# Performance work log

Measured on AMD Instinct MI355X. Metric: run time of the kernel, lower is better.

## Reference

```python
import jax, jax.numpy as jnp
import numpy as np

F = 32          # conf['num_features']
G = 96          # voxel grid extent
N_VOX = 80000   # occupied input voxels
BN_EPS = 1e-5


def _encode(c):
    c = c.astype(np.int64) + 8
    return (c[:, 0] * 512 + c[:, 1]) * 512 + c[:, 2]


def _offsets(ks, dil):
    r = np.arange(-(ks // 2), ks // 2 + 1) * dil
    return np.stack(np.meshgrid(r, r, r, indexing='ij'), -1).reshape(-1, 3)


def _build_map(in_coords, out_coords, offsets):
    # For each kernel offset k and output voxel j, find input voxel index at
    # out_coords[j] + offsets[k]; sentinel = n_in / n_out when absent.
    n_in, n_out = len(in_coords), len(out_coords)
    keys = _encode(in_coords)
    order = np.argsort(keys).astype(np.int32)
    skeys = keys[order]
    K = len(offsets)
    in_map = np.full((K, n_out), n_in, np.int32)
    out_map = np.full((K, n_out), n_out, np.int32)
    base = np.arange(n_out, dtype=np.int32)
    for k, off in enumerate(offsets):
        q = _encode(out_coords + off)
        pos = np.clip(np.searchsorted(skeys, q), 0, n_in - 1)
        valid = skeys[pos] == q
        in_map[k] = np.where(valid, order[pos], n_in)
        out_map[k] = np.where(valid, base, n_out)
    return jnp.asarray(in_map), jnp.asarray(out_map)


def setup_inputs() -> dict:
    rng = np.random.default_rng(0)
    idx = rng.choice(G ** 3, size=N_VOX, replace=False)
    coords = np.stack(np.unravel_index(idx, (G, G, G)), 1).astype(np.int64)
    c2 = np.unique(coords // 2 * 2, axis=0)   # stride-2 coords (enc1 output)
    c4 = np.unique(coords // 4 * 4, axis=0)   # stride-4 coords (c_out.C)

    m1_in, m1_out = _build_map(coords, c2, _offsets(5, 1))  # k5 s2 conv
    m2_in, m2_out = _build_map(c2, c2, _offsets(3, 2))      # enc1 blocks
    m3_in, m3_out = _build_map(c2, c4, _offsets(3, 2))      # conv2 -> c_out.C
    m4_in, m4_out = _build_map(c4, c4, _offsets(3, 4))      # enc2 blocks

    key = jax.random.key(0)
    ks = jax.random.split(key, 8)
    s = 0.05
    return {
        'x_geo': jax.random.normal(ks[0], (N_VOX, 1), jnp.float32),
        'x_col': jax.random.uniform(ks[1], (N_VOX, 3), jnp.float32),
        'w0': jax.random.normal(ks[2], (125, 4, F), jnp.float32) * s,
        'w_e1': jax.random.normal(ks[3], (2, 2, 27, F, F), jnp.float32) * s,
        'g_e1': jnp.ones((2, 2, F), jnp.float32),
        'b_e1': jnp.zeros((2, 2, F), jnp.float32),
        'w2': jax.random.normal(ks[4], (27, F, 2 * F), jnp.float32) * s,
        'w_e2': jax.random.normal(ks[5], (2, 2, 27, 2 * F, 2 * F), jnp.float32) * s,
        'g_e2': jnp.ones((2, 2, 2 * F), jnp.float32),
        'b_e2': jnp.zeros((2, 2, 2 * F), jnp.float32),
        'm1_in': m1_in, 'm1_out': m1_out,
        'm2_in': m2_in, 'm2_out': m2_out,
        'm3_in': m3_in, 'm3_out': m3_out,
        'm4_in': m4_in, 'm4_out': m4_out,
    }


def sparse_conv(feats, W, in_map, out_map):
    # gather -> GEMM -> scatter per kernel offset (lax.scan over K offsets)
    n_out = out_map.shape[1]
    fpad = jnp.concatenate([feats, jnp.zeros((1, feats.shape[1]), feats.dtype)], 0)
    out0 = jnp.zeros((n_out + 1, W.shape[2]), feats.dtype)
    def step(acc, kmw):
        im, om, w = kmw
        return acc.at[om].add(fpad[im] @ w), None
    out, _ = jax.lax.scan(step, out0, (in_map, out_map, W))
    return out[:n_out]


def batch_norm(x, g, b):
    mu = x.mean(0)
    var = ((x - mu) ** 2).mean(0)
    return (x - mu) * jax.lax.rsqrt(var + BN_EPS) * g + b


def basic_block(x, w, g, b, in_map, out_map):
    # ME BasicBlock: conv-BN-ReLU-conv-BN + residual, ReLU
    y = jax.nn.relu(batch_norm(sparse_conv(x, w[0], in_map, out_map), g[0], b[0]))
    y = batch_norm(sparse_conv(y, w[1], in_map, out_map), g[1], b[1])
    return jax.nn.relu(y + x)


def reference(x_geo, x_col, w0, w_e1, g_e1, b_e1, w2, w_e2, g_e2, b_e2,
              m1_in, m1_out, m2_in, m2_out, m3_in, m3_out, m4_in, m4_out):
    x = jnp.concatenate([x_geo, x_col], axis=1)          # ME.cat -> 4 channels
    x = jax.nn.relu(sparse_conv(x, w0, m1_in, m1_out))   # k5 s2 conv + ReLU
    for i in range(2):                                   # enc1 residual blocks
        x = basic_block(x, w_e1[i], g_e1[i], b_e1[i], m2_in, m2_out)
    x = sparse_conv(x, w2, m3_in, m3_out)                # conv2 onto c_out.C
    for i in range(2):                                   # enc2 residual blocks
        x = basic_block(x, w_e2[i], g_e2[i], b_e2[i], m4_in, m4_out)
    return x
```

## Files before the change

kernel.cpp:

```cpp
#include <hip/hip_runtime.h>
#include <hip/hip_bf16.h>


typedef float f4 __attribute__((ext_vector_type(4)));
typedef short short8 __attribute__((ext_vector_type(8)));
typedef short short4v __attribute__((ext_vector_type(4)));

#define BN_EPS 1e-5f

static inline int ceil_div(int a, int b) { return (a + b - 1) / b; }

static __device__ inline float btof(short s) {
    unsigned u = ((unsigned)(unsigned short)s) << 16;
    float f;
    __builtin_memcpy(&f, &u, 4);
    return f;
}
static __device__ inline short ftob(float f) {
    __hip_bfloat16 h = __float2bfloat16(f);
    short s;
    __builtin_memcpy(&s, &h, 2);
    return s;
}

static __device__ inline int xcd_swz(int b, int nwg) {
    int q = nwg >> 3, rr = nwg & 7;
    int xcd = b & 7, pos = b >> 3;
    return (xcd < rr) ? (xcd * (q + 1) + pos)
                      : (rr * (q + 1) + (xcd - rr) * q + pos);
}

static __device__ inline void gl_lds16(const void* g, void* l) {
    __builtin_amdgcn_global_load_lds(
        (const __attribute__((address_space(1))) void*)g,
        (__attribute__((address_space(3))) void*)l, 16, 0, 0);
}

template <int N>
static __device__ inline void s_wait_vmcnt() {
    static_assert(N >= 0 && N <= 20, "vmcnt range");
    if constexpr (N == 0) asm volatile("s_waitcnt vmcnt(0)" ::: "memory");
    else if constexpr (N == 8) asm volatile("s_waitcnt vmcnt(8)" ::: "memory");
    else if constexpr (N == 9) asm volatile("s_waitcnt vmcnt(9)" ::: "memory");
    else if constexpr (N == 18) asm volatile("s_waitcnt vmcnt(18)" ::: "memory");
    else if constexpr (N == 6) asm volatile("s_waitcnt vmcnt(6)" ::: "memory");
    else asm volatile("s_waitcnt vmcnt(4)" ::: "memory");
}

struct Seg {
    const float* W;
    long long begin, end;
    int K, CIN, COUT;
};

struct ProArgs {
    Seg s[10];
    const float* geo;
    const float* col;
    __hip_bfloat16* x0;
    int n_vox;
    float* stats;
    __hip_bfloat16* pads[5];
    int padn[5];
    long long wf_total;
    long long pro_total;
    __hip_bfloat16* Wf;
    const int* m1;
    __hip_bfloat16* A;
    int nc2;
};

template <int C>
__device__ inline void bn_coef(const float* st, const float* g, const float* b,
                               int c, int n, float& sc, float& sh) {
    constexpr int NS = (C == 32) ? 8 : 4;
    float rn = 1.f / (float)n;
    float sum = 0.f, sq = 0.f;
#pragma unroll
    for (int s = 0; s < NS; ++s) {
        sum += st[(s * 2 + 0) * C + c];
        sq  += st[(s * 2 + 1) * C + c];
    }
    float mu = sum * rn;
    float inv = rsqrtf(sq * rn - mu * mu + BN_EPS);
    sc = inv * g[c];
    sh = b[c] - mu * sc;
}

__global__ __launch_bounds__(256) void k_prologue(ProArgs pa) {
    for (long long e = (long long)blockIdx.x * 256 + threadIdx.x; e < pa.pro_total;
         e += (long long)gridDim.x * 256) {
        if (e < pa.wf_total) {
            int si = 0;
#pragma unroll
            for (int i = 0; i < 10; ++i)
                if (e >= pa.s[i].end) si = i + 1;
            const Seg sg = pa.s[si];
            long long r = e - sg.begin;
            int j = (int)(r & 7);
            int lane = (int)((r >> 3) & 63);
            long long rest = r >> 9;
            int NT = sg.COUT >> 4;
            int ntile = (int)(rest % NT);
            int chunk = (int)(rest / NT);
            int kd = chunk * 32 + ((lane >> 4) << 3) + j;
            int koff = kd / sg.CIN;
            int ci = kd % sg.CIN;
            int n = ntile * 16 + (lane & 15);
            float v = (koff < sg.K) ? sg.W[((size_t)koff * sg.CIN + ci) * sg.COUT + n] : 0.f;
            pa.Wf[e] = __float2bfloat16(v);
            continue;
        }
        long long r = e - pa.wf_total;
        if (r < pa.n_vox) {
            int row = (int)r;
            pa.x0[row * 4 + 0] = __float2bfloat16(pa.geo[row]);
            pa.x0[row * 4 + 1] = __float2bfloat16(pa.col[row * 3 + 0]);
            pa.x0[row * 4 + 2] = __float2bfloat16(pa.col[row * 3 + 1]);
            pa.x0[row * 4 + 3] = __float2bfloat16(pa.col[row * 3 + 2]);
            continue;
        }
        r -= pa.n_vox;
        if (r < 4096) {
            pa.stats[r] = 0.f;
            continue;
        }
        r -= 4096;
#pragma unroll
        for (int i = 0; i < 5; ++i) {
            if (r < pa.padn[i]) {
                pa.pads[i][r] = __float2bfloat16(0.f);
                r = -1;
                break;
            }
            r -= pa.padn[i];
        }
    }
}

__global__ __launch_bounds__(256) void k_stem(ProArgs a) {
    const int t = threadIdx.x, w = t >> 6, lane = t & 63;
    const int quad = lane >> 4, ml = lane & 15;
    const int ntile = w & 1, mgroup = w >> 1;
    const int n_out = a.nc2, n_in = a.n_vox;
    const __hip_bfloat16* feat = a.x0;
    const __hip_bfloat16* Wf = a.Wf;
    const int* in_map = a.m1;
    __hip_bfloat16* out = a.A;
    const int mb = blockIdx.x * 64 + mgroup * 32;
    const int m0 = mb + ml, m1 = mb + 16 + ml;
    const bool v0 = m0 < n_out, v1 = m1 < n_out;
    f4 acc0 = {0.f, 0.f, 0.f, 0.f};
    f4 acc1 = {0.f, 0.f, 0.f, 0.f};
#pragma unroll 2
    for (int chunk = 0; chunk < 16; ++chunk) {
        int k0 = chunk * 8 + quad * 2;
        int k1 = k0 + 1;
        int k0c = (k0 < 125) ? k0 : 0;
        int k1c = (k1 < 125) ? k1 : 0;
        short8 b = *(const short8*)(Wf + ((size_t)(chunk * 2 + ntile) * 64 + lane) * 8);
        int ia = v0 ? in_map[(size_t)k0c * n_out + m0] : n_in;
        int ib = v0 ? in_map[(size_t)k1c * n_out + m0] : n_in;
        int ic = v1 ? in_map[(size_t)k0c * n_out + m1] : n_in;
        int id = v1 ? in_map[(size_t)k1c * n_out + m1] : n_in;
        short4v p0 = *(const short4v*)(feat + (size_t)ia * 4);
        short4v p1 = *(const short4v*)(feat + (size_t)ib * 4);
        short4v p2 = *(const short4v*)(feat + (size_t)ic * 4);
        short4v p3 = *(const short4v*)(feat + (size_t)id * 4);
        short8 a0, a1;
        a0[0] = p0[0]; a0[1] = p0[1]; a0[2] = p0[2]; a0[3] = p0[3];
        a0[4] = p1[0]; a0[5] = p1[1]; a0[6] = p1[2]; a0[7] = p1[3];
        a1[0] = p2[0]; a1[1] = p2[1]; a1[2] = p2[2]; a1[3] = p2[3];
        a1[4] = p3[0]; a1[5] = p3[1]; a1[6] = p3[2]; a1[7] = p3[3];
        acc0 = __builtin_amdgcn_mfma_f32_16x16x32_bf16(a0, b, acc0, 0, 0, 0);
        acc1 = __builtin_amdgcn_mfma_f32_16x16x32_bf16(a1, b, acc1, 0, 0, 0);
    }
    const int col = ntile * 16 + ml;
#pragma unroll
    for (int i = 0; i < 4; ++i) {
        int r0 = mb + quad * 4 + i;
        if (r0 < n_out)
            out[(size_t)r0 * 32 + col] = __float2bfloat16(fmaxf(acc0[i], 0.f));
        int r1 = mb + 16 + quad * 4 + i;
        if (r1 < n_out)
            out[(size_t)r1 * 32 + col] = __float2bfloat16(fmaxf(acc1[i], 0.f));
    }
}

template <int CIN, int COUT, int MT, int K, bool BNF>
__global__ __launch_bounds__(256, (CIN == 64) ? 3 : 4)
void k_conv(
    const __hip_bfloat16* __restrict__ feat,
    const __hip_bfloat16* __restrict__ Wf,
    const int* __restrict__ in_map,
    __hip_bfloat16* __restrict__ out,
    float* __restrict__ stats,
    const float* __restrict__ in_stats,
    const float* __restrict__ in_g,
    const float* __restrict__ in_b,
    int n_out, int n_in) {
    constexpr int NT = COUT / 16;
    constexpr int H = CIN / 32;
    constexpr int R = MT * 16;
    constexpr int KPW = (K + 3) / 4;
    constexpr int SP = COUT + 1;
    constexpr int S = CIN / 8;
    constexpr int SW = (S == 4) ? 1 : 0;
    constexpr int RPI = 64 / S;
    constexpr int NI = R / RPI;
    constexpr int NB = H * NT;
    constexpr int D = 2;
    constexpr int WAIT_N = NI + 2 * NB;
    constexpr int NSLOT = (COUT == 32) ? 8 : 4;
    constexpr int STAGE_B = R * CIN * 2;
    constexpr int STAGE_TOT = 4 * D * STAGE_B;
    constexpr int RED_B = 4 * R * SP * 4;
    constexpr int UNION_B = (STAGE_TOT > RED_B) ? STAGE_TOT : RED_B;

    __shared__ char smem[UNION_B + 2048 + 512];
    float* red  = (float*)smem;
    float* sred = (float*)(smem + UNION_B);
    float* ibn  = (float*)(smem + UNION_B + 2048);

    const int t = threadIdx.x, w = t >> 6, lane = t & 63;
    const int quad = lane >> 4, ml = lane & 15;
    const int wb = xcd_swz((int)blockIdx.x, (int)gridDim.x);
    const int mb = wb * R;
    char* stw = smem + w * (D * STAGE_B);
    const int srow = lane / S;
    const int ssl = lane & (S - 1);

    if constexpr (BNF) {
        if (t < CIN) {
            float sc, sh;
            bn_coef<CIN>(in_stats, in_g, in_b, t, n_in, sc, sh);
            ibn[t] = sc;
            ibn[CIN + t] = sh;
        }
        __syncthreads();
    }
    float scr[H][8], shr[H][8];
    if constexpr (BNF) {
#pragma unroll
        for (int h = 0; h < H; ++h)
#pragma unroll
            for (int j = 0; j < 8; ++j) {
                int ch = h * 32 + quad * 8 + j;
                scr[h][j] = ibn[ch];
                shr[h][j] = ibn[CIN + ch];
            }
    }

    int idxs[KPW][NI];
#pragma unroll
    for (int kk = 0; kk < KPW; ++kk) {
        const int k = kk * 4 + w;
        const int krow = (k < K) ? k : 0;
        const int* mk = in_map + (size_t)krow * n_out;
#pragma unroll
        for (int inst = 0; inst < NI; ++inst) {
            int m = mb + inst * RPI + srow;
            idxs[kk][inst] = (m < n_out) ? mk[m] : n_in;
        }
    }

    f4 acc[MT * NT];
#pragma unroll
    for (int i = 0; i < MT * NT; ++i) acc[i] = (f4){0.f, 0.f, 0.f, 0.f};

    short8 bf0[NB], bf1[NB];

    auto issue_stage = [&](int stg, int slot) {
#pragma unroll
        for (int inst = 0; inst < NI; ++inst) {
            int rg = inst * RPI + srow;
            int gsl = ssl ^ ((rg >> SW) & (S - 1));
            const __hip_bfloat16* src =
                feat + (size_t)idxs[stg][inst] * CIN + gsl * 8;
            gl_lds16(src, stw + slot * STAGE_B + inst * 1024);
        }
    };
    auto issue_bf = [&](int stg, short8 (&bfc)[NB]) {
        const int k = stg * 4 + w;
#pragma unroll
        for (int h = 0; h < H; ++h)
#pragma unroll
            for (int nt = 0; nt < NT; ++nt)
                bfc[h * NT + nt] = *(const short8*)(
                    Wf + (((size_t)(k * H + h) * NT + nt) * 64 + lane) * 8);
    };

    issue_stage(0, 0);
    issue_bf(0, bf0);
    issue_stage(1, 1);
    issue_bf(1, bf1);
    __builtin_amdgcn_sched_barrier(0);

#pragma unroll
    for (int kk = 0; kk < KPW; ++kk) {
        s_wait_vmcnt<WAIT_N>();
        __builtin_amdgcn_sched_barrier(0);

        const int slot = kk & 1;
        short8 (&bfc)[NB] = (kk & 1) ? bf1 : bf0;

        int cidx[MT];
        if constexpr (BNF) {
#pragma unroll
            for (int mi = 0; mi < MT; ++mi) {
                if constexpr (RPI >= 16) {
                    cidx[mi] = __shfl(idxs[kk][(mi * 16) / RPI], ml * S);
                } else {
                    int a0 = __shfl(idxs[kk][0], (ml & 7) * S);
                    int a1 = __shfl(idxs[kk][NI - 1], (ml & 7) * S);
                    cidx[mi] = (ml < 8) ? a0 : a1;
                }
            }
        }

#pragma unroll
        for (int mi = 0; mi < MT; ++mi) {
#pragma unroll
            for (int h = 0; h < H; ++h) {
                const int p = (h * 4 + quad) ^ ((ml >> SW) & (S - 1));
                short8 a = *(const short8*)(
                    stw + slot * STAGE_B + ((mi * 16 + ml) * CIN + p * 8) * 2);
                if constexpr (BNF) {
                    const bool sent = (cidx[mi] == n_in);
#pragma unroll
                    for (int j = 0; j < 8; ++j) {
                        float f = btof(a[j]) * scr[h][j] + shr[h][j];
                        f = fmaxf(f, 0.f);
                        a[j] = sent ? (short)0 : ftob(f);
                    }
                }
#pragma unroll
                for (int nt = 0; nt < NT; ++nt)
                    acc[mi * NT + nt] = __builtin_amdgcn_mfma_f32_16x16x32_bf16(
                        a, bfc[h * NT + nt], acc[mi * NT + nt], 0, 0, 0);
            }
        }

        __builtin_amdgcn_sched_barrier(0);
        const int ns = (kk + 2 < KPW) ? (kk + 2) : 0;
        issue_stage(ns, slot);
        if (kk & 1) issue_bf(ns, bf1); else issue_bf(ns, bf0);
        __builtin_amdgcn_sched_barrier(0);
    }

#pragma unroll
    for (int i = 0; i < NB; ++i) {
        asm volatile("" ::"v"(bf0[i]));
        asm volatile("" ::"v"(bf1[i]));
    }

    s_wait_vmcnt<0>();
    __syncthreads();

#pragma unroll
    for (int mi = 0; mi < MT; ++mi)
#pragma unroll
        for (int nt = 0; nt < NT; ++nt)
#pragma unroll
            for (int i = 0; i < 4; ++i)
                red[((size_t)w * R + mi * 16 + quad * 4 + i) * SP + nt * 16 + ml] =
                    acc[mi * NT + nt][i];
    __syncthreads();

    constexpr int E = (R * COUT) / 256;
    constexpr int RSTEP = 256 / COUT;
    const int col = t % COUT;
    const int rg = t / COUT;
    float s = 0.f, s2 = 0.f;
#pragma unroll
    for (int i = 0; i < E; ++i) {
        int r = rg + i * RSTEP;
        float v = red[(0 * R + r) * SP + col] + red[(1 * R + r) * SP + col] +
                  red[(2 * R + r) * SP + col] + red[(3 * R + r) * SP + col];
        s += v;
        s2 += v * v;
        int grow = mb + r;
        if (grow < n_out) out[(size_t)grow * COUT + col] = __float2bfloat16(v);
    }

    if (stats) {
        sred[t] = s;
        sred[256 + t] = s2;
        __syncthreads();
        if (t < 2 * COUT) {
            int c = t % COUT;
            int which = t / COUT;
            float v = 0.f;
#pragma unroll
            for (int j = 0; j < RSTEP; ++j) v += sred[which * 256 + j * COUT + c];
            atomicAdd(&stats[((wb & (NSLOT - 1)) * 2 + which) * COUT + c], v);
        }
    }
}

template <int C, bool F32OUT>
__global__ __launch_bounds__(256) void k_bnres(
    const __hip_bfloat16* __restrict__ y, const __hip_bfloat16* __restrict__ res,
    const float* __restrict__ st, const float* __restrict__ g,
    const float* __restrict__ b, void* outp, int n) {
    __shared__ float ibn[2 * C];
    const int t = threadIdx.x;
    if (t < C) {
        float sc, sh;
        bn_coef<C>(st, g, b, t, n, sc, sh);
        ibn[t] = sc;
        ibn[C + t] = sh;
    }
    __syncthreads();
    long long tot = (long long)n * (C / 8);
    long long i = (long long)blockIdx.x * 256 + t;
    if (i >= tot) return;
    int c0 = (int)(i % (C / 8)) * 8;
    short8 v = *(const short8*)(y + i * 8);
    short8 r = *(const short8*)(res + i * 8);
    if constexpr (F32OUT) {
        float* out = (float*)outp;
        f4 o0, o1;
#pragma unroll
        for (int j = 0; j < 8; ++j) {
            float f = btof(v[j]) * ibn[c0 + j] + ibn[C + c0 + j] + btof(r[j]);
            f = fmaxf(f, 0.f);
            if (j < 4) o0[j] = f; else o1[j - 4] = f;
        }
        *(f4*)(out + i * 8) = o0;
        *(f4*)(out + i * 8 + 4) = o1;
    } else {
        __hip_bfloat16* out = (__hip_bfloat16*)outp;
        short8 o;
#pragma unroll
        for (int j = 0; j < 8; ++j) {
            float f = btof(v[j]) * ibn[c0 + j] + ibn[C + c0 + j] + btof(r[j]);
            o[j] = ftob(fmaxf(f, 0.f));
        }
        *(short8*)(out + i * 8) = o;
    }
}

extern "C" void kernel_launch(void* const* d_in, const int* in_sizes, int n_in_cnt,
                              void* d_out, int out_size, void* d_ws, size_t ws_size,
                              hipStream_t stream) {
    const float* x_geo = (const float*)d_in[0];
    const float* x_col = (const float*)d_in[1];
    const float* w0    = (const float*)d_in[2];
    const float* w_e1  = (const float*)d_in[3];
    const float* g_e1  = (const float*)d_in[4];
    const float* b_e1  = (const float*)d_in[5];
    const float* w2    = (const float*)d_in[6];
    const float* w_e2  = (const float*)d_in[7];
    const float* g_e2  = (const float*)d_in[8];
    const float* b_e2  = (const float*)d_in[9];
    const int* m1 = (const int*)d_in[10];
    const int* m2 = (const int*)d_in[12];
    const int* m3 = (const int*)d_in[14];
    const int* m4 = (const int*)d_in[16];

    const int n_vox = in_sizes[0];
    const int nc2 = in_sizes[10] / 125;
    const int nc4 = in_sizes[14] / 27;
    (void)out_size; (void)ws_size; (void)n_in_cnt;

    char* p = (char*)d_ws;
    auto alloc = [&](size_t bytes) -> char* {
        char* r = p;
        p += (bytes + 255) & ~(size_t)255;
        return r;
    };
    float* stats = (float*)alloc(8 * 512 * sizeof(float));
    __hip_bfloat16* x0 = (__hip_bfloat16*)alloc((size_t)(n_vox + 1) * 4 * 2);
    __hip_bfloat16* A  = (__hip_bfloat16*)alloc((size_t)(nc2 + 1) * 32 * 2);
    __hip_bfloat16* B  = (__hip_bfloat16*)alloc((size_t)(nc2 + 1) * 32 * 2);
    __hip_bfloat16* Cb = (__hip_bfloat16*)alloc((size_t)(nc2 + 1) * 32 * 2);
    __hip_bfloat16* D  = (__hip_bfloat16*)alloc((size_t)(nc4 + 1) * 64 * 2);
    __hip_bfloat16* E  = (__hip_bfloat16*)alloc((size_t)(nc4 + 1) * 64 * 2);
    __hip_bfloat16* Fb = (__hip_bfloat16*)alloc((size_t)(nc4 + 1) * 64 * 2);

    const long long sz_stem = 16LL * 2 * 512;
    const long long sz_e1   = 28LL * 2 * 512;
    const long long sz_c2   = 28LL * 4 * 512;
    const long long sz_e2   = 56LL * 4 * 512;
    const long long wf_total = sz_stem + 4 * sz_e1 + sz_c2 + 4 * sz_e2;
    __hip_bfloat16* Wf = (__hip_bfloat16*)alloc((size_t)wf_total * 2);

    ProArgs pa;
    long long cur = 0;
    auto seg = [&](int i, const float* W, int K, int CIN, int COUT, long long n) {
        pa.s[i].W = W; pa.s[i].K = K; pa.s[i].CIN = CIN; pa.s[i].COUT = COUT;
        pa.s[i].begin = cur; pa.s[i].end = cur + n; cur += n;
    };
    seg(0, w0, 125, 4, 32, sz_stem);
    for (int i = 0; i < 4; ++i)
        seg(1 + i, w_e1 + (size_t)i * 27 * 32 * 32, 27, 32, 32, sz_e1);
    seg(5, w2, 27, 32, 64, sz_c2);
    for (int i = 0; i < 4; ++i)
        seg(6 + i, w_e2 + (size_t)i * 27 * 64 * 64, 27, 64, 64, sz_e2);

    long long off_e1[4], off_e2[4];
    cur = sz_stem;
    for (int i = 0; i < 4; ++i) { off_e1[i] = cur; cur += sz_e1; }
    long long off_c2 = cur; cur += sz_c2;
    for (int i = 0; i < 4; ++i) { off_e2[i] = cur; cur += sz_e2; }

    pa.geo = x_geo; pa.col = x_col; pa.x0 = x0; pa.n_vox = n_vox;
    pa.stats = stats;
    pa.pads[0] = x0 + (size_t)n_vox * 4; pa.padn[0] = 4;
    pa.pads[1] = A + (size_t)nc2 * 32;   pa.padn[1] = 32;
    pa.pads[2] = B + (size_t)nc2 * 32;   pa.padn[2] = 32;
    pa.pads[3] = D + (size_t)nc4 * 64;   pa.padn[3] = 64;
    pa.pads[4] = E + (size_t)nc4 * 64;   pa.padn[4] = 64;
    pa.wf_total = wf_total;
    pa.pro_total = wf_total + n_vox + 4096 + (4 + 32 + 32 + 64 + 64);
    pa.Wf = Wf;
    pa.m1 = m1;
    pa.A = A;
    pa.nc2 = nc2;

    k_prologue<<<ceil_div((int)pa.pro_total, 256), 256, 0, stream>>>(pa);
    k_stem<<<ceil_div(nc2, 64), 256, 0, stream>>>(pa);

    k_conv<32, 32, 4, 27, false><<<ceil_div(nc2, 64), 256, 0, stream>>>(
        A, Wf + off_e1[0], m2, B, stats + 0 * 512,
        nullptr, nullptr, nullptr, nc2, nc2);
    k_conv<32, 32, 4, 27, true><<<ceil_div(nc2, 64), 256, 0, stream>>>(
        B, Wf + off_e1[1], m2, Cb, stats + 1 * 512,
        stats + 0 * 512, g_e1 + 0, b_e1 + 0, nc2, nc2);
    k_bnres<32, false><<<ceil_div(nc2 * 4, 256), 256, 0, stream>>>(
        Cb, A, stats + 1 * 512, g_e1 + 32, b_e1 + 32, A, nc2);

    k_conv<32, 32, 4, 27, false><<<ceil_div(nc2, 64), 256, 0, stream>>>(
        A, Wf + off_e1[2], m2, B, stats + 2 * 512,
        nullptr, nullptr, nullptr, nc2, nc2);
    k_conv<32, 32, 4, 27, true><<<ceil_div(nc2, 64), 256, 0, stream>>>(
        B, Wf + off_e1[3], m2, Cb, stats + 3 * 512,
        stats + 2 * 512, g_e1 + 64, b_e1 + 64, nc2, nc2);
    k_bnres<32, false><<<ceil_div(nc2 * 4, 256), 256, 0, stream>>>(
        Cb, A, stats + 3 * 512, g_e1 + 96, b_e1 + 96, A, nc2);

    k_conv<32, 64, 1, 27, false><<<ceil_div(nc4, 16), 256, 0, stream>>>(
        A, Wf + off_c2, m3, D, nullptr,
        nullptr, nullptr, nullptr, nc4, nc2);

    k_conv<64, 64, 1, 27, false><<<ceil_div(nc4, 16), 256, 0, stream>>>(
        D, Wf + off_e2[0], m4, E, stats + 4 * 512,
        nullptr, nullptr, nullptr, nc4, nc4);
    k_conv<64, 64, 1, 27, true><<<ceil_div(nc4, 16), 256, 0, stream>>>(
        E, Wf + off_e2[1], m4, Fb, stats + 5 * 512,
        stats + 4 * 512, g_e2 + 0, b_e2 + 0, nc4, nc4);
    k_bnres<64, false><<<ceil_div(nc4 * 8, 256), 256, 0, stream>>>(
        Fb, D, stats + 5 * 512, g_e2 + 64, b_e2 + 64, D, nc4);

    k_conv<64, 64, 1, 27, false><<<ceil_div(nc4, 16), 256, 0, stream>>>(
        D, Wf + off_e2[2], m4, E, stats + 6 * 512,
        nullptr, nullptr, nullptr, nc4, nc4);
    k_conv<64, 64, 1, 27, true><<<ceil_div(nc4, 16), 256, 0, stream>>>(
        E, Wf + off_e2[3], m4, Fb, stats + 7 * 512,
        stats + 6 * 512, g_e2 + 128, b_e2 + 128, nc4, nc4);
    k_bnres<64, true><<<ceil_div(nc4 * 8, 256), 256, 0, stream>>>(
        Fb, D, stats + 7 * 512, g_e2 + 192, b_e2 + 192, (float*)d_out, nc4);
}
```

Before: 306.9 us.

## Add hybrid LDS/register gather schedule for MT=4 enc1 conv; shift-based prologue indexing

For the enc1 conv shape (MT==4), kernel offsets now alternate between two paths. Even stages gather rows into LDS with global_load_lds, and odd stages load rows straight into registers in MFMA layout, with a deeper prefetch of four steps ahead. The aim is to cut LDS staging traffic and hide gather latency better, at the cost of more VGPRs; occupancy is lowered to 3 waves for this shape. The prologue weight reformat also replaces integer div/mod with shifts and masks, using log2 fields added per segment.

New measurement: 320.3 us. 4.4% more time.

```diff
diff --git a/kernel.cpp b/kernel.cpp
--- a/kernel.cpp
+++ b/kernel.cpp
@@ -38,19 +38,19 @@
 
 template <int N>
 static __device__ inline void s_wait_vmcnt() {
-    static_assert(N >= 0 && N <= 20, "vmcnt range");
     if constexpr (N == 0) asm volatile("s_waitcnt vmcnt(0)" ::: "memory");
+    else if constexpr (N == 6) asm volatile("s_waitcnt vmcnt(6)" ::: "memory");
+    else if constexpr (N == 9) asm volatile("s_waitcnt vmcnt(9)" ::: "memory");
+    else if constexpr (N == 14) asm volatile("s_waitcnt vmcnt(14)" ::: "memory");
+    else if constexpr (N == 18) asm volatile("s_waitcnt vmcnt(18)" ::: "memory");
     else if constexpr (N == 8) asm volatile("s_waitcnt vmcnt(8)" ::: "memory");
-    else if constexpr (N == 9) asm volatile("s_waitcnt vmcnt(9)" ::: "memory");
-    else if constexpr (N == 18) asm volatile("s_waitcnt vmcnt(18)" ::: "memory");
-    else if constexpr (N == 6) asm volatile("s_waitcnt vmcnt(6)" ::: "memory");
     else asm volatile("s_waitcnt vmcnt(4)" ::: "memory");
 }
 
 struct Seg {
     const float* W;
     long long begin, end;
-    int K, CIN, COUT;
+    int K, CIN, COUT, lgc, lgnt;
 };
 
 struct ProArgs {
@@ -100,12 +100,11 @@
             int j = (int)(r & 7);
             int lane = (int)((r >> 3) & 63);
             long long rest = r >> 9;
-            int NT = sg.COUT >> 4;
-            int ntile = (int)(rest % NT);
-            int chunk = (int)(rest / NT);
+            int ntile = (int)(rest & ((1 << sg.lgnt) - 1));
+            int chunk = (int)(rest >> sg.lgnt);
             int kd = chunk * 32 + ((lane >> 4) << 3) + j;
-            int koff = kd / sg.CIN;
-            int ci = kd % sg.CIN;
+            int koff = kd >> sg.lgc;
+            int ci = kd & (sg.CIN - 1);
             int n = ntile * 16 + (lane & 15);
             float v = (koff < sg.K) ? sg.W[((size_t)koff * sg.CIN + ci) * sg.COUT + n] : 0.f;
             pa.Wf[e] = __float2bfloat16(v);
@@ -188,7 +187,7 @@
 }
 
 template <int CIN, int COUT, int MT, int K, bool BNF>
-__global__ __launch_bounds__(256, (CIN == 64) ? 3 : 4)
+__global__ __launch_bounds__(256, (CIN == 64 || MT == 4) ? 3 : 4)
 void k_conv(
     const __hip_bfloat16* __restrict__ feat,
     const __hip_bfloat16* __restrict__ Wf,
@@ -216,6 +215,9 @@
     constexpr int STAGE_TOT = 4 * D * STAGE_B;
     constexpr int RED_B = 4 * R * SP * 4;
     constexpr int UNION_B = (STAGE_TOT > RED_B) ? STAGE_TOT : RED_B;
+    constexpr bool HYB = (MT == 4);
+    static_assert(!HYB || (NI == 4 && NB == 2 && H == 1 && KPW == 7),
+                  "hybrid schedule assumes enc1 shape");
 
     __shared__ char smem[UNION_B + 2048 + 512];
     float* red  = (float*)smem;
@@ -251,111 +253,250 @@
             }
     }
 
-    int idxs[KPW][NI];
-#pragma unroll
-    for (int kk = 0; kk < KPW; ++kk) {
-        const int k = kk * 4 + w;
-        const int krow = (k < K) ? k : 0;
-        const int* mk = in_map + (size_t)krow * n_out;
-#pragma unroll
-        for (int inst = 0; inst < NI; ++inst) {
-            int m = mb + inst * RPI + srow;
-            idxs[kk][inst] = (m < n_out) ? mk[m] : n_in;
-        }
-    }
-
     f4 acc[MT * NT];
 #pragma unroll
     for (int i = 0; i < MT * NT; ++i) acc[i] = (f4){0.f, 0.f, 0.f, 0.f};
 
-    short8 bf0[NB], bf1[NB];
-
-    auto issue_stage = [&](int stg, int slot) {
-#pragma unroll
-        for (int inst = 0; inst < NI; ++inst) {
-            int rg = inst * RPI + srow;
-            int gsl = ssl ^ ((rg >> SW) & (S - 1));
-            const __hip_bfloat16* src =
-                feat + (size_t)idxs[stg][inst] * CIN + gsl * 8;
-            gl_lds16(src, stw + slot * STAGE_B + inst * 1024);
-        }
-    };
-    auto issue_bf = [&](int stg, short8 (&bfc)[NB]) {
-        const int k = stg * 4 + w;
-#pragma unroll
-        for (int h = 0; h < H; ++h)
+    if constexpr (HYB) {
+        int sidx[4][NI];
+        int vidx[3][MT];
+#pragma unroll
+        for (int e = 0; e < 4; ++e) {
+            const int k = (2 * e) * 4 + w;
+            const int krow = (k < K) ? k : 0;
+            const int* mk = in_map + (size_t)krow * n_out;
+#pragma unroll
+            for (int inst = 0; inst < NI; ++inst) {
+                int m = mb + inst * RPI + srow;
+                sidx[e][inst] = (m < n_out) ? mk[m] : n_in;
+            }
+        }
+#pragma unroll
+        for (int o = 0; o < 3; ++o) {
+            const int k = (2 * o + 1) * 4 + w;
+            const int krow = (k < K) ? k : 0;
+            const int* mk = in_map + (size_t)krow * n_out;
+#pragma unroll
+            for (int mi = 0; mi < MT; ++mi) {
+                int m = mb + mi * 16 + ml;
+                vidx[o][mi] = (m < n_out) ? mk[m] : n_in;
+            }
+        }
+
+        short8 vs0[MT], vs1[MT];
+        short8 bf0[NB], bf1[NB];
+
+        auto issue_S = [&](int e, int slot) {
+#pragma unroll
+            for (int inst = 0; inst < NI; ++inst) {
+                int rg = inst * RPI + srow;
+                int gsl = ssl ^ ((rg >> SW) & (S - 1));
+                const __hip_bfloat16* src =
+                    feat + (size_t)sidx[e][inst] * CIN + gsl * 8;
+                gl_lds16(src, stw + slot * STAGE_B + inst * 1024);
+            }
+        };
+        auto issue_V = [&](int o, short8 (&vs)[MT]) {
+#pragma unroll
+            for (int mi = 0; mi < MT; ++mi)
+                vs[mi] = *(const short8*)(
+                    feat + (size_t)vidx[o][mi] * CIN + quad * 8);
+        };
+        auto issue_B = [&](int kk, short8 (&bfc)[NB]) {
+            const int k = kk * 4 + w;
+#pragma unroll
+            for (int h = 0; h < H; ++h)
+#pragma unroll
+                for (int nt = 0; nt < NT; ++nt)
+                    bfc[h * NT + nt] = *(const short8*)(
+                        Wf + (((size_t)(k * H + h) * NT + nt) * 64 + lane) * 8);
+        };
+        auto mfma_row = [&](int mi, short8 a, short8 (&bfc)[NB], bool sent) {
+            if constexpr (BNF) {
+#pragma unroll
+                for (int j = 0; j < 8; ++j) {
+                    float f = btof(a[j]) * scr[0][j] + shr[0][j];
+                    f = fmaxf(f, 0.f);
+                    a[j] = sent ? (short)0 : ftob(f);
+                }
+            }
+            (void)sent;
 #pragma unroll
             for (int nt = 0; nt < NT; ++nt)
-                bfc[h * NT + nt] = *(const short8*)(
-                    Wf + (((size_t)(k * H + h) * NT + nt) * 64 + lane) * 8);
-    };
-
-    issue_stage(0, 0);
-    issue_bf(0, bf0);
-    issue_stage(1, 1);
-    issue_bf(1, bf1);
-    __builtin_amdgcn_sched_barrier(0);
-
-#pragma unroll
-    for (int kk = 0; kk < KPW; ++kk) {
-        s_wait_vmcnt<WAIT_N>();
+                acc[mi * NT + nt] = __builtin_amdgcn_mfma_f32_16x16x32_bf16(
+                    a, bfc[nt], acc[mi * NT + nt], 0, 0, 0);
+        };
+
+        issue_S(0, 0);
+        issue_B(0, bf0);
+        issue_V(0, vs0);
+        issue_B(1, bf1);
+        issue_S(1, 1);
+        issue_V(1, vs1);
         __builtin_amdgcn_sched_barrier(0);
 
-        const int slot = kk & 1;
-        short8 (&bfc)[NB] = (kk & 1) ? bf1 : bf0;
-
-        int cidx[MT];
-        if constexpr (BNF) {
-#pragma unroll
-            for (int mi = 0; mi < MT; ++mi) {
-                if constexpr (RPI >= 16) {
-                    cidx[mi] = __shfl(idxs[kk][(mi * 16) / RPI], ml * S);
-                } else {
-                    int a0 = __shfl(idxs[kk][0], (ml & 7) * S);
-                    int a1 = __shfl(idxs[kk][NI - 1], (ml & 7) * S);
-                    cidx[mi] = (ml < 8) ? a0 : a1;
+#pragma unroll
+        for (int kk = 0; kk < 7; ++kk) {
+            if (kk < 2) s_wait_vmcnt<14>(); else s_wait_vmcnt<6>();
+            __builtin_amdgcn_sched_barrier(0);
+
+            if ((kk & 1) == 0) {
+                const int e = kk >> 1;
+                const int slot = e & 1;
+                int cidx[MT];
+                if constexpr (BNF) {
+#pragma unroll
+                    for (int mi = 0; mi < MT; ++mi)
+                        cidx[mi] = __shfl(sidx[e][mi], ml * S);
                 }
-            }
-        }
-
-#pragma unroll
-        for (int mi = 0; mi < MT; ++mi) {
-#pragma unroll
-            for (int h = 0; h < H; ++h) {
-                const int p = (h * 4 + quad) ^ ((ml >> SW) & (S - 1));
-                short8 a = *(const short8*)(
-                    stw + slot * STAGE_B + ((mi * 16 + ml) * CIN + p * 8) * 2);
-                if constexpr (BNF) {
-                    const bool sent = (cidx[mi] == n_in);
-#pragma unroll
-                    for (int j = 0; j < 8; ++j) {
-                        float f = btof(a[j]) * scr[h][j] + shr[h][j];
-                        f = fmaxf(f, 0.f);
-                        a[j] = sent ? (short)0 : ftob(f);
+#pragma unroll
+                for (int mi = 0; mi < MT; ++mi) {
+                    const int p = quad ^ ((ml >> SW) & (S - 1));
+                    short8 a = *(const short8*)(
+                        stw + slot * STAGE_B + ((mi * 16 + ml) * CIN + p * 8) * 2);
+                    bool sent = false;
+                    if constexpr (BNF) sent = (cidx[mi] == n_in);
+                    if (kk & 1) mfma_row(mi, a, bf1, sent);
+                    else        mfma_row(mi, a, bf0, sent);
+                }
+            } else {
+                const int o = kk >> 1;
+#pragma unroll
+                for (int mi = 0; mi < MT; ++mi) {
+                    short8 a = (o & 1) ? vs1[mi] : vs0[mi];
+                    bool sent = false;
+                    if constexpr (BNF) sent = (vidx[o][mi] == n_in);
+                    mfma_row(mi, a, bf1, sent);
+                }
+            }
+
+            __builtin_amdgcn_sched_barrier(0);
+            const int nk = kk + 4;
+            if ((nk & 1) == 0) {
+                issue_S((nk <= 6) ? (nk >> 1) : 0, (nk >> 1) & 1);
+            } else {
+                const int no = (nk <= 5) ? (nk >> 1) : 0;
+                if ((nk >> 1) & 1) issue_V(no, vs1); else issue_V(no, vs0);
+            }
+            const int nbk = (kk + 2 <= 6) ? (kk + 2) : 0;
+            if ((kk + 2) & 1) issue_B(nbk, bf1); else issue_B(nbk, bf0);
+            __builtin_amdgcn_sched_barrier(0);
+        }
+
+#pragma unroll
+        for (int i = 0; i < NB; ++i) {
+            asm volatile("" ::"v"(bf0[i]));
+            asm volatile("" ::"v"(bf1[i]));
+        }
+#pragma unroll
+        for (int i = 0; i < MT; ++i) {
+            asm volatile("" ::"v"(vs0[i]));
+            asm volatile("" ::"v"(vs1[i]));
+        }
+        s_wait_vmcnt<0>();
+        __syncthreads();
+    } else {
+        int idxs[KPW][NI];
+#pragma unroll
+        for (int kk = 0; kk < KPW; ++kk) {
+            const int k = kk * 4 + w;
+            const int krow = (k < K) ? k : 0;
+            const int* mk = in_map + (size_t)krow * n_out;
+#pragma unroll
+            for (int inst = 0; inst < NI; ++inst) {
+                int m = mb + inst * RPI + srow;
+                idxs[kk][inst] = (m < n_out) ? mk[m] : n_in;
+            }
+        }
+
+        short8 bf0[NB], bf1[NB];
+
+        auto issue_stage = [&](int stg, int slot) {
+#pragma unroll
+            for (int inst = 0; inst < NI; ++inst) {
+                int rg = inst * RPI + srow;
+                int gsl = ssl ^ ((rg >> SW) & (S - 1));
+                const __hip_bfloat16* src =
+                    feat + (size_t)idxs[stg][inst] * CIN + gsl * 8;
+                gl_lds16(src, stw + slot * STAGE_B + inst * 1024);
+            }
+        };
+        auto issue_bf = [&](int stg, short8 (&bfc)[NB]) {
+            const int k = stg * 4 + w;
+#pragma unroll
+            for (int h = 0; h < H; ++h)
+#pragma unroll
+                for (int nt = 0; nt < NT; ++nt)
+                    bfc[h * NT + nt] = *(const short8*)(
+                        Wf + (((size_t)(k * H + h) * NT + nt) * 64 + lane) * 8);
+        };
+
+        issue_stage(0, 0);
+        issue_bf(0, bf0);
+        issue_stage(1, 1);
+        issue_bf(1, bf1);
+        __builtin_amdgcn_sched_barrier(0);
+
+#pragma unroll
+        for (int kk = 0; kk < KPW; ++kk) {
+            s_wait_vmcnt<WAIT_N>();
+            __builtin_amdgcn_sched_barrier(0);
+
+            const int slot = kk & 1;
+            short8 (&bfc)[NB] = (kk & 1) ? bf1 : bf0;
+
+            int cidx[MT];
+            if constexpr (BNF) {
+#pragma unroll
+                for (int mi = 0; mi < MT; ++mi) {
+                    if constexpr (RPI >= 16) {
+                        cidx[mi] = __shfl(idxs[kk][(mi * 16) / RPI], ml * S);
+                    } else {
+                        int a0 = __shfl(idxs[kk][0], (ml & 7) * S);
+                        int a1 = __shfl(idxs[kk][NI - 1], (ml & 7) * S);
+                        cidx[mi] = (ml < 8) ? a0 : a1;
                     }
                 }
-#pragma unroll
-                for (int nt = 0; nt < NT; ++nt)
-                    acc[mi * NT + nt] = __builtin_amdgcn_mfma_f32_16x16x32_bf16(
-                        a, bfc[h * NT + nt], acc[mi * NT + nt], 0, 0, 0);
-            }
-        }
-
-        __builtin_amdgcn_sched_barrier(0);
-        const int ns = (kk + 2 < KPW) ? (kk + 2) : 0;
-        issue_stage(ns, slot);
-        if (kk & 1) issue_bf(ns, bf1); else issue_bf(ns, bf0);
-        __builtin_amdgcn_sched_barrier(0);
-    }
-
-#pragma unroll
-    for (int i = 0; i < NB; ++i) {
-        asm volatile("" ::"v"(bf0[i]));
-        asm volatile("" ::"v"(bf1[i]));
-    }
-
-    s_wait_vmcnt<0>();
-    __syncthreads();
+            }
+
+#pragma unroll
+            for (int mi = 0; mi < MT; ++mi) {
+#pragma unroll
+                for (int h = 0; h < H; ++h) {
+                    const int p = (h * 4 + quad) ^ ((ml >> SW) & (S - 1));
+                    short8 a = *(const short8*)(
+                        stw + slot * STAGE_B + ((mi * 16 + ml) * CIN + p * 8) * 2);
+                    if constexpr (BNF) {
+                        const bool sent = (cidx[mi] == n_in);
+#pragma unroll
+                        for (int j = 0; j < 8; ++j) {
+                            float f = btof(a[j]) * scr[h][j] + shr[h][j];
+                            f = fmaxf(f, 0.f);
+                            a[j] = sent ? (short)0 : ftob(f);
+                        }
+                    }
+#pragma unroll
+                    for (int nt = 0; nt < NT; ++nt)
+                        acc[mi * NT + nt] = __builtin_amdgcn_mfma_f32_16x16x32_bf16(
+                            a, bfc[h * NT + nt], acc[mi * NT + nt], 0, 0, 0);
+                }
+            }
+
+            __builtin_amdgcn_sched_barrier(0);
+            const int ns = (kk + 2 < KPW) ? (kk + 2) : 0;
+            issue_stage(ns, slot);
+            if (kk & 1) issue_bf(ns, bf1); else issue_bf(ns, bf0);
+            __builtin_amdgcn_sched_barrier(0);
+        }
+
+#pragma unroll
+        for (int i = 0; i < NB; ++i) {
+            asm volatile("" ::"v"(bf0[i]));
+            asm volatile("" ::"v"(bf1[i]));
+        }
+        s_wait_vmcnt<0>();
+        __syncthreads();
+    }
 
 #pragma unroll
     for (int mi = 0; mi < MT; ++mi)
@@ -490,6 +631,8 @@
     long long cur = 0;
     auto seg = [&](int i, const float* W, int K, int CIN, int COUT, long long n) {
         pa.s[i].W = W; pa.s[i].K = K; pa.s[i].CIN = CIN; pa.s[i].COUT = COUT;
+        pa.s[i].lgc = (CIN == 4) ? 2 : (CIN == 32) ? 5 : 6;
+        pa.s[i].lgnt = (COUT == 32) ? 1 : 2;
         pa.s[i].begin = cur; pa.s[i].end = cur + n; cur += n;
     };
     seg(0, w0, 125, 4, 32, sz_stem);
```
